# Kernel optimization log

Measured on AMD Instinct MI355X. Metric: run time of the kernel, lower is better.

The kernel has to match this reference:

```python
import jax, jax.numpy as jnp
import numpy as np

B, NB, K, L, S, V = 32, 688, 4, 688, 688, 50
PAD = 0
TEMP = 0.1
SMOOTH = 0.1
L_CLS, L_PTR, L_EMPTY, L_ROW, L_COL = 1.0, 1.0, 1.0, 0.5, 0.5


def setup_inputs() -> dict:
    key = jax.random.key(0)
    ks = jax.random.split(key, 12)
    tag_logits = jax.random.normal(ks[0], (B, S, V), jnp.float32)
    tag_targets = jax.random.randint(ks[1], (B, S), 0, V)
    pointer_logits = jax.random.normal(ks[2], (B, NB, S), jnp.float32)
    # targets only on even OTSL positions (which we mark as data tags below)
    raw = jax.random.randint(ks[3], (B, NB, K), 0, S // 2) * 2
    drop = jax.random.uniform(ks[4], (B, NB, K)) < 0.25
    box_indices = jnp.where(drop, -1, raw)
    pos = jnp.arange(S)
    data_otsl = jnp.broadcast_to(pos % 2 == 0, (B, S))
    empty_otsl = (pos % 2 == 1)[None, :] & (jax.random.uniform(ks[5], (B, S)) < 0.5)
    zeros_prompt = jnp.zeros((B, L), bool)
    data_tag_mask = jnp.concatenate([zeros_prompt, data_otsl], axis=1)
    empty_tag_mask = jnp.concatenate([zeros_prompt, empty_otsl], axis=1)
    empty_pointer_logits = jax.random.normal(ks[6], (B, 1, S), jnp.float32)
    row_sim_matrix = jax.random.normal(ks[7], (B, NB, NB), jnp.float32)
    col_sim_matrix = jax.random.normal(ks[8], (B, NB, NB), jnp.float32)

    def make_coef(k):
        k1, k2 = jax.random.split(k)
        c = jax.random.uniform(k1, (B, NB, NB))
        inv = jax.random.uniform(k2, (B, NB, NB)) < 0.1
        return jnp.where(inv, -1.0, c)

    row_span_coef = make_coef(ks[9])
    col_span_coef = make_coef(ks[10])
    return dict(tag_logits=tag_logits, tag_targets=tag_targets,
                pointer_logits=pointer_logits, box_indices=box_indices,
                data_tag_mask=data_tag_mask, empty_tag_mask=empty_tag_mask,
                empty_pointer_logits=empty_pointer_logits,
                row_sim_matrix=row_sim_matrix, col_sim_matrix=col_sim_matrix,
                row_span_coef=row_span_coef, col_span_coef=col_span_coef)


def _tag_loss(tag_logits, tag_targets):
    logp = jax.nn.log_softmax(tag_logits, axis=-1).reshape(-1, V)
    t = tag_targets.reshape(-1)
    valid = t != PAD
    nll = -jnp.take_along_axis(logp, jnp.where(valid, t, 0)[:, None], axis=1)[:, 0]
    smooth = -logp.mean(axis=-1)
    per = (1.0 - SMOOTH) * nll + SMOOTH * smooth
    return (per * valid).sum() / valid.sum()


def _pointer_loss(pointer_logits, box_indices, data_tag_mask):
    log_probs = jax.nn.log_softmax(pointer_logits / TEMP, axis=-1)  # (B,NB,S)
    valid_pos = data_tag_mask[:, L:]  # (B,S)
    log_probs = jnp.where(valid_pos[:, None, :], log_probs, -jnp.inf)
    valid = box_indices != -1  # (B,NB,K)
    safe = jnp.where(valid, box_indices, 0)
    g = jnp.take_along_axis(log_probs, safe, axis=-1)  # (B,NB,K)
    g = jnp.where(valid, g, 0.0)
    cnt = valid.sum(axis=-1)  # (B,NB)
    has = cnt > 0
    per = -(g.sum(axis=-1) / jnp.maximum(cnt, 1))
    total = (per * has).sum()
    return total / (has.sum() + 1e-6)


def _empty_ptr_loss(empty_logits, data_tag_mask, empty_tag_mask):
    x = empty_logits[:, 0, :]  # (B,S)
    otsl_mask = (data_tag_mask | empty_tag_mask)[:, L:]
    targets = empty_tag_mask[:, L:].astype(jnp.float32)
    # stable BCE with logits
    bce = jnp.maximum(x, 0.0) - x * targets + jnp.log1p(jnp.exp(-jnp.abs(x)))
    masked = bce * otsl_mask
    num_c = otsl_mask.sum(axis=1) + 1e-08
    return (masked.sum(axis=1) / num_c).mean()


def _contrastive_loss(sim, coef):
    s = sim / TEMP
    e = jnp.exp(s)
    lp = jnp.log(e / e.sum(axis=-1, keepdims=True) + 1e-08)
    vm = coef >= 0
    w = coef * lp * vm
    box = -(w.sum(axis=-1) / (coef.sum(axis=-1) + 1e-08))
    vb = vm.any(axis=-1)
    return (box * vb).sum() / (vb.sum() + 1e-08)


def reference(tag_logits, tag_targets, pointer_logits, box_indices,
              data_tag_mask, empty_tag_mask, empty_pointer_logits,
              row_sim_matrix, col_sim_matrix, row_span_coef, col_span_coef):
    cls_loss = _tag_loss(tag_logits, tag_targets)
    ptr_loss = _pointer_loss(pointer_logits, box_indices, data_tag_mask)
    empty_loss = _empty_ptr_loss(empty_pointer_logits, data_tag_mask, empty_tag_mask)
    row_loss = _contrastive_loss(row_sim_matrix, row_span_coef)
    col_loss = _contrastive_loss(col_sim_matrix, col_span_coef)
    total = (L_CLS * cls_loss + L_PTR * ptr_loss + L_EMPTY * empty_loss
             + L_ROW * row_loss + L_COL * col_loss)
    return (total, cls_loss, ptr_loss, empty_loss, row_loss, col_loss)
```

## Files before the change

### kernel.cpp

```cpp
#include <hip/hip_runtime.h>
#include <cstddef>

namespace {

constexpr int B  = 32;
constexpr int NB = 688;
constexpr int K  = 4;
constexpr int L  = 688;
constexpr int S  = 688;
constexpr int V  = 50;
constexpr int LS = L + S;
constexpr int ROWS = B * NB;
constexpr float TINV = 10.0f;
constexpr int Q3 = S / 4 - 128;
constexpr int QR = S / 4;

constexpr int NBLK  = 1024;
constexpr int NWAVE = NBLK * 4;

constexpr int A_PT = 0, A_PH = 1, A_RS = 2, A_RV = 3, A_CS = 4,
              A_CV = 5, A_TS = 6, A_TC = 7, A_ES = 8;

__device__ __forceinline__ float wred_sum(float v) {
#pragma unroll
  for (int o = 32; o > 0; o >>= 1) v += __shfl_xor(v, o);
  return v;
}
__device__ __forceinline__ void wred2(float& a, float& b) {
#pragma unroll
  for (int o = 32; o > 0; o >>= 1) { a += __shfl_xor(a, o); b += __shfl_xor(b, o); }
}
__device__ __forceinline__ void wred4(float& a, float& b, float& c, float& d) {
#pragma unroll
  for (int o = 32; o > 0; o >>= 1) {
    a += __shfl_xor(a, o); b += __shfl_xor(b, o);
    c += __shfl_xor(c, o); d += __shfl_xor(d, o);
  }
}

__device__ __forceinline__ float4 q_exp_t(const float4 v) {
  return make_float4(__expf(v.x * TINV), __expf(v.y * TINV),
                     __expf(v.z * TINV), __expf(v.w * TINV));
}
__device__ __forceinline__ float q_sum(const float4 a) {
  return (a.x + a.y) + (a.z + a.w);
}

__device__ __forceinline__ void load3(const float4* __restrict__ p4, int lane,
                                      bool t3, float4& a, float4& b, float4& c) {
  a = p4[lane];
  b = p4[lane + 64];
  c = t3 ? p4[lane + 128] : make_float4(0.f, 0.f, 0.f, 0.f);
}

__device__ __forceinline__ void c_quad(const float4 e, const float4 c,
                                       float A, float lgz,
                                       float& wsum, float& csum, bool& anyv) {
  csum += ((c.x + c.y) + (c.z + c.w));
  if (c.x >= 0.f) { wsum += c.x * (__logf(e.x + A) - lgz); anyv = true; }
  if (c.y >= 0.f) { wsum += c.y * (__logf(e.y + A) - lgz); anyv = true; }
  if (c.z >= 0.f) { wsum += c.z * (__logf(e.z + A) - lgz); anyv = true; }
  if (c.w >= 0.f) { wsum += c.w * (__logf(e.w + A) - lgz); anyv = true; }
}

__device__ __forceinline__ void ptr_row(int r, int lane, bool t3,
    const float* __restrict__ plog, const int* __restrict__ box,
    const int* __restrict__ dmask, float& a0, float& a1)
{
  const float*  pl  = plog + (size_t)r * S;
  const float4* pl4 = reinterpret_cast<const float4*>(pl);
  float4 v0, v1, v2;
  load3(pl4, lane, t3, v0, v1, v2);
  int idx = (lane < K) ? box[(size_t)r * K + lane] : -1;

  float4 e0 = q_exp_t(v0);
  float4 e1 = q_exp_t(v1);
  float4 e2 = t3 ? q_exp_t(v2) : make_float4(0.f, 0.f, 0.f, 0.f);
  float z = q_sum(e0) + q_sum(e1) + q_sum(e2);
  z = wred_sum(z);
  float lse = __logf(z);

  bool vld = (idx != -1) & (lane < K);
  float g = 0.f;
  if (vld) {
    int bb = r / NB;
    int vp = dmask[(size_t)bb * LS + L + idx];
    float sv = pl[idx] * TINV;
    g = vp ? (sv - lse) : -INFINITY;
  }
  g += __shfl_xor(g, 1);
  g += __shfl_xor(g, 2);
  unsigned long long bal = __ballot(vld);
  int cnt = __popcll(bal);
  if (cnt > 0) {
    a0 += -(g / (float)cnt);
    a1 += 1.f;
  }
}

__device__ __forceinline__ void tag_row(int row, int lane,
    const float* __restrict__ tl_base, const int* __restrict__ tgt,
    float& a0, float& a1)
{
  const float* tl = tl_base + (size_t)row * V;
  const bool a = (lane < V);
  float xv = a ? tl[lane] : 0.f;
  int   t  = tgt[row];
  float ev = a ? __expf(xv) : 0.f;
  float sx = a ? xv : 0.f;
  wred2(ev, sx);
  float lse = __logf(ev);
  float xt  = __shfl(xv, t);
  if (t != 0) {
    a0 += lse - 0.9f * xt - 0.002f * sx;
    a1 += 1.f;
  }
}

__device__ __forceinline__ void empty_row(int b, int lane,
    const float* __restrict__ elog, const int* __restrict__ dmask,
    const int* __restrict__ emask, float& a0)
{
  const float* el = elog + (size_t)b * S;
  const int* dm = dmask + (size_t)b * LS + L;
  const int* em = emask + (size_t)b * LS + L;
  float bs = 0.f, bc = 0.f;
  for (int j = lane; j < S; j += 64) {
    float xv = el[j];
    int d = dm[j], e = em[j];
    float tt = (float)e;
    float bce = fmaxf(xv, 0.f) - xv * tt + log1pf(__expf(-fabsf(xv)));
    if (d | e) { bs += bce; bc += 1.f; }
  }
  wred2(bs, bc);
  a0 += bs / (bc + 1e-8f);
}

__global__ __launch_bounds__(256, 4) void fused_loss(
    const float* __restrict__ tag_logits, const int* __restrict__ tag_targets,
    const float* __restrict__ plog, const int* __restrict__ box,
    const int* __restrict__ dmask, const int* __restrict__ emask,
    const float* __restrict__ elog,
    const float* __restrict__ rsim, const float* __restrict__ csim,
    const float* __restrict__ rcoef, const float* __restrict__ ccoef,
    float* __restrict__ ws)
{
  const int tid  = threadIdx.x;
  const int lane = tid & 63;
  const int wave = tid >> 6;
  const int wid  = blockIdx.x * 4 + wave;
  const bool t3  = (lane < Q3);

  const int ws_ = (wid * 43) >> 3;
  const int we_ = ((wid + 1) * 43) >> 3;

  float aPT = 0.f, aPH = 0.f, aRS = 0.f, aRV = 0.f, aCS = 0.f,
        aCV = 0.f, aTS = 0.f, aTC = 0.f, aES = 0.f;

  {
    float4 nr0, nr1, nr2, nm0, nm1, nm2;
    int r = ws_;
    if (r < we_) {
      load3(reinterpret_cast<const float4*>(rsim) + (size_t)r * QR, lane, t3, nr0, nr1, nr2);
      load3(reinterpret_cast<const float4*>(csim) + (size_t)r * QR, lane, t3, nm0, nm1, nm2);
    }
    while (r < we_) {
      float4 x0 = nr0, x1 = nr1, x2 = nr2;
      float4 y0 = nm0, y1 = nm1, y2 = nm2;
      float4 cr0, cr1, cr2, cm0, cm1, cm2;
      load3(reinterpret_cast<const float4*>(rcoef) + (size_t)r * QR, lane, t3, cr0, cr1, cr2);
      load3(reinterpret_cast<const float4*>(ccoef) + (size_t)r * QR, lane, t3, cm0, cm1, cm2);
      const int rn = r + 1;
      if (rn < we_) {
        load3(reinterpret_cast<const float4*>(rsim) + (size_t)rn * QR, lane, t3, nr0, nr1, nr2);
        load3(reinterpret_cast<const float4*>(csim) + (size_t)rn * QR, lane, t3, nm0, nm1, nm2);
      }
      x0 = q_exp_t(x0); x1 = q_exp_t(x1);
      x2 = t3 ? q_exp_t(x2) : make_float4(0.f, 0.f, 0.f, 0.f);
      y0 = q_exp_t(y0); y1 = q_exp_t(y1);
      y2 = t3 ? q_exp_t(y2) : make_float4(0.f, 0.f, 0.f, 0.f);

      float zr = q_sum(x0) + q_sum(x1) + q_sum(x2);
      float zc = q_sum(y0) + q_sum(y1) + q_sum(y2);
      wred2(zr, zc);
      const float Ar = 1e-8f * zr, lgzr = __logf(zr);
      const float Ac = 1e-8f * zc, lgzc = __logf(zc);

      float wr = 0.f, cr = 0.f, wc = 0.f, cc = 0.f;
      bool anyr = false, anyc = false;
      c_quad(x0, cr0, Ar, lgzr, wr, cr, anyr);
      c_quad(y0, cm0, Ac, lgzc, wc, cc, anyc);
      c_quad(x1, cr1, Ar, lgzr, wr, cr, anyr);
      c_quad(y1, cm1, Ac, lgzc, wc, cc, anyc);
      if (t3) {
        c_quad(x2, cr2, Ar, lgzr, wr, cr, anyr);
        c_quad(y2, cm2, Ac, lgzc, wc, cc, anyc);
      }
      wred4(wr, cr, wc, cc);
      if (__ballot(anyr)) { aRS += -(wr / (cr + 1e-8f)); aRV += 1.f; }
      if (__ballot(anyc)) { aCS += -(wc / (cc + 1e-8f)); aCV += 1.f; }
      r = rn;
    }
  }

  for (int r = ws_; r < we_; ++r) {
    ptr_row(r, lane, t3, plog, box, dmask, aPT, aPH);
    tag_row(r, lane, tag_logits, tag_targets, aTS, aTC);
  }

  if (wid < B) empty_row(wid, lane, elog, dmask, emask, aES);

  if (lane == 0) {
    ws[A_PT * NWAVE + wid] = aPT;
    ws[A_PH * NWAVE + wid] = aPH;
    ws[A_RS * NWAVE + wid] = aRS;
    ws[A_RV * NWAVE + wid] = aRV;
    ws[A_CS * NWAVE + wid] = aCS;
    ws[A_CV * NWAVE + wid] = aCV;
    ws[A_TS * NWAVE + wid] = aTS;
    ws[A_TC * NWAVE + wid] = aTC;
    ws[A_ES * NWAVE + wid] = aES;
  }
}

__global__ __launch_bounds__(256) void combine_kernel(
    const float* __restrict__ ws, float* __restrict__ out)
{
  const int tid  = threadIdx.x;
  const int lane = tid & 63;
  const int w    = tid >> 6;
  double acc[9];
#pragma unroll
  for (int a = 0; a < 9; ++a) acc[a] = 0.0;
  for (int i = tid; i < NWAVE; i += 256) {
#pragma unroll
    for (int a = 0; a < 9; ++a) acc[a] += (double)ws[a * NWAVE + i];
  }
#pragma unroll
  for (int a = 0; a < 9; ++a) {
#pragma unroll
    for (int o = 32; o > 0; o >>= 1) acc[a] += __shfl_xor(acc[a], o);
  }
  __shared__ double sh[4][9];
  if (lane == 0) {
#pragma unroll
    for (int a = 0; a < 9; ++a) sh[w][a] = acc[a];
  }
  __syncthreads();
  if (tid == 0) {
    double t[9];
#pragma unroll
    for (int a = 0; a < 9; ++a) t[a] = sh[0][a] + sh[1][a] + sh[2][a] + sh[3][a];
    float cls  = (float)(t[A_TS] / t[A_TC]);
    float ptr  = (float)(t[A_PT] / (t[A_PH] + 1e-6));
    float emp  = (float)(t[A_ES] / (double)B);
    float row  = (float)(t[A_RS] / (t[A_RV] + 1e-8));
    float col  = (float)(t[A_CS] / (t[A_CV] + 1e-8));
    float total = cls + ptr + emp + 0.5f * row + 0.5f * col;
    out[0] = total; out[1] = cls; out[2] = ptr;
    out[3] = emp;   out[4] = row; out[5] = col;
  }
}

}

extern "C" void kernel_launch(void* const* d_in, const int* in_sizes, int n_in,
                              void* d_out, int out_size, void* d_ws, size_t ws_size,
                              hipStream_t stream)
{
  const float* tag_logits  = (const float*)d_in[0];
  const int*   tag_targets = (const int*)  d_in[1];
  const float* plog        = (const float*)d_in[2];
  const int*   box         = (const int*)  d_in[3];
  const int*   dmask       = (const int*)  d_in[4];
  const int*   emask       = (const int*)  d_in[5];
  const float* elog        = (const float*)d_in[6];
  const float* rsim        = (const float*)d_in[7];
  const float* csim        = (const float*)d_in[8];
  const float* rcoef       = (const float*)d_in[9];
  const float* ccoef       = (const float*)d_in[10];

  float* ws  = (float*)d_ws;
  float* out = (float*)d_out;

  fused_loss<<<NBLK, 256, 0, stream>>>(tag_logits, tag_targets, plog, box,
                                       dmask, emask, elog, rsim, csim,
                                       rcoef, ccoef, ws);
  combine_kernel<<<1, 256, 0, stream>>>(ws, out);
}
```

Measured before the change: 72.37 us.

## Software-pipeline pointer/tag rows, use nontemporal loads and exp2, reduce per block

Fuses the pointer and tag row loops into one loop that prefetches the next row's pointer logits, box indices and tag logits while computing the current row, and merges their wave reductions into a single three-way shuffle reduction. The contrastive loads become nontemporal, and exp(x*10) is computed as exp2 with a folded constant. Per-wave partials are now summed in shared memory and written once per block, which shrinks the workspace the combine kernel reads. The prefetching raises register pressure, and the per-block reduction adds a block-wide barrier.

```diff
diff --git a/kernel.cpp b/kernel.cpp
--- a/kernel.cpp
+++ b/kernel.cpp
@@ -10,25 +10,32 @@
 constexpr int S  = 688;
 constexpr int V  = 50;
 constexpr int LS = L + S;
-constexpr int ROWS = B * NB;
 constexpr float TINV = 10.0f;
+constexpr float E10  = 14.4269504088896340736f;
 constexpr int Q3 = S / 4 - 128;
 constexpr int QR = S / 4;
 
 constexpr int NBLK  = 1024;
 constexpr int NWAVE = NBLK * 4;
 
+typedef float f32x4 __attribute__((ext_vector_type(4)));
+
 constexpr int A_PT = 0, A_PH = 1, A_RS = 2, A_RV = 3, A_CS = 4,
               A_CV = 5, A_TS = 6, A_TC = 7, A_ES = 8;
 
-__device__ __forceinline__ float wred_sum(float v) {
-#pragma unroll
-  for (int o = 32; o > 0; o >>= 1) v += __shfl_xor(v, o);
-  return v;
+__device__ __forceinline__ f32x4 zero4() {
+  f32x4 z = {0.f, 0.f, 0.f, 0.f};
+  return z;
 }
 __device__ __forceinline__ void wred2(float& a, float& b) {
 #pragma unroll
   for (int o = 32; o > 0; o >>= 1) { a += __shfl_xor(a, o); b += __shfl_xor(b, o); }
+}
+__device__ __forceinline__ void wred3(float& a, float& b, float& c) {
+#pragma unroll
+  for (int o = 32; o > 0; o >>= 1) {
+    a += __shfl_xor(a, o); b += __shfl_xor(b, o); c += __shfl_xor(c, o);
+  }
 }
 __device__ __forceinline__ void wred4(float& a, float& b, float& c, float& d) {
 #pragma unroll
@@ -38,22 +45,25 @@
   }
 }
 
-__device__ __forceinline__ float4 q_exp_t(const float4 v) {
-  return make_float4(__expf(v.x * TINV), __expf(v.y * TINV),
-                     __expf(v.z * TINV), __expf(v.w * TINV));
-}
-__device__ __forceinline__ float q_sum(const float4 a) {
+__device__ __forceinline__ f32x4 q_exp10(const f32x4 v) {
+  f32x4 r;
+  r.x = exp2f(v.x * E10); r.y = exp2f(v.y * E10);
+  r.z = exp2f(v.z * E10); r.w = exp2f(v.w * E10);
+  return r;
+}
+__device__ __forceinline__ float q_sum(const f32x4 a) {
   return (a.x + a.y) + (a.z + a.w);
 }
 
-__device__ __forceinline__ void load3(const float4* __restrict__ p4, int lane,
-                                      bool t3, float4& a, float4& b, float4& c) {
-  a = p4[lane];
-  b = p4[lane + 64];
-  c = t3 ? p4[lane + 128] : make_float4(0.f, 0.f, 0.f, 0.f);
-}
-
-__device__ __forceinline__ void c_quad(const float4 e, const float4 c,
+__device__ __forceinline__ void load3nt(const f32x4* __restrict__ p4, int lane,
+                                        bool t3, f32x4& a, f32x4& b, f32x4& c) {
+  a = __builtin_nontemporal_load(p4 + lane);
+  b = __builtin_nontemporal_load(p4 + lane + 64);
+  c = zero4();
+  if (t3) c = __builtin_nontemporal_load(p4 + lane + 128);
+}
+
+__device__ __forceinline__ void c_quad(const f32x4 e, const f32x4 c,
                                        float A, float lgz,
                                        float& wsum, float& csum, bool& anyv) {
   csum += ((c.x + c.y) + (c.z + c.w));
@@ -61,60 +71,6 @@
   if (c.y >= 0.f) { wsum += c.y * (__logf(e.y + A) - lgz); anyv = true; }
   if (c.z >= 0.f) { wsum += c.z * (__logf(e.z + A) - lgz); anyv = true; }
   if (c.w >= 0.f) { wsum += c.w * (__logf(e.w + A) - lgz); anyv = true; }
-}
-
-__device__ __forceinline__ void ptr_row(int r, int lane, bool t3,
-    const float* __restrict__ plog, const int* __restrict__ box,
-    const int* __restrict__ dmask, float& a0, float& a1)
-{
-  const float*  pl  = plog + (size_t)r * S;
-  const float4* pl4 = reinterpret_cast<const float4*>(pl);
-  float4 v0, v1, v2;
-  load3(pl4, lane, t3, v0, v1, v2);
-  int idx = (lane < K) ? box[(size_t)r * K + lane] : -1;
-
-  float4 e0 = q_exp_t(v0);
-  float4 e1 = q_exp_t(v1);
-  float4 e2 = t3 ? q_exp_t(v2) : make_float4(0.f, 0.f, 0.f, 0.f);
-  float z = q_sum(e0) + q_sum(e1) + q_sum(e2);
-  z = wred_sum(z);
-  float lse = __logf(z);
-
-  bool vld = (idx != -1) & (lane < K);
-  float g = 0.f;
-  if (vld) {
-    int bb = r / NB;
-    int vp = dmask[(size_t)bb * LS + L + idx];
-    float sv = pl[idx] * TINV;
-    g = vp ? (sv - lse) : -INFINITY;
-  }
-  g += __shfl_xor(g, 1);
-  g += __shfl_xor(g, 2);
-  unsigned long long bal = __ballot(vld);
-  int cnt = __popcll(bal);
-  if (cnt > 0) {
-    a0 += -(g / (float)cnt);
-    a1 += 1.f;
-  }
-}
-
-__device__ __forceinline__ void tag_row(int row, int lane,
-    const float* __restrict__ tl_base, const int* __restrict__ tgt,
-    float& a0, float& a1)
-{
-  const float* tl = tl_base + (size_t)row * V;
-  const bool a = (lane < V);
-  float xv = a ? tl[lane] : 0.f;
-  int   t  = tgt[row];
-  float ev = a ? __expf(xv) : 0.f;
-  float sx = a ? xv : 0.f;
-  wred2(ev, sx);
-  float lse = __logf(ev);
-  float xt  = __shfl(xv, t);
-  if (t != 0) {
-    a0 += lse - 0.9f * xt - 0.002f * sx;
-    a1 += 1.f;
-  }
 }
 
 __device__ __forceinline__ void empty_row(int b, int lane,
@@ -158,27 +114,27 @@
         aCV = 0.f, aTS = 0.f, aTC = 0.f, aES = 0.f;
 
   {
-    float4 nr0, nr1, nr2, nm0, nm1, nm2;
+    f32x4 nr0, nr1, nr2, nm0, nm1, nm2;
     int r = ws_;
     if (r < we_) {
-      load3(reinterpret_cast<const float4*>(rsim) + (size_t)r * QR, lane, t3, nr0, nr1, nr2);
-      load3(reinterpret_cast<const float4*>(csim) + (size_t)r * QR, lane, t3, nm0, nm1, nm2);
+      load3nt(reinterpret_cast<const f32x4*>(rsim) + (size_t)r * QR, lane, t3, nr0, nr1, nr2);
+      load3nt(reinterpret_cast<const f32x4*>(csim) + (size_t)r * QR, lane, t3, nm0, nm1, nm2);
     }
     while (r < we_) {
-      float4 x0 = nr0, x1 = nr1, x2 = nr2;
-      float4 y0 = nm0, y1 = nm1, y2 = nm2;
-      float4 cr0, cr1, cr2, cm0, cm1, cm2;
-      load3(reinterpret_cast<const float4*>(rcoef) + (size_t)r * QR, lane, t3, cr0, cr1, cr2);
-      load3(reinterpret_cast<const float4*>(ccoef) + (size_t)r * QR, lane, t3, cm0, cm1, cm2);
+      f32x4 x0 = nr0, x1 = nr1, x2 = nr2;
+      f32x4 y0 = nm0, y1 = nm1, y2 = nm2;
+      f32x4 cr0, cr1, cr2, cm0, cm1, cm2;
+      load3nt(reinterpret_cast<const f32x4*>(rcoef) + (size_t)r * QR, lane, t3, cr0, cr1, cr2);
+      load3nt(reinterpret_cast<const f32x4*>(ccoef) + (size_t)r * QR, lane, t3, cm0, cm1, cm2);
       const int rn = r + 1;
       if (rn < we_) {
-        load3(reinterpret_cast<const float4*>(rsim) + (size_t)rn * QR, lane, t3, nr0, nr1, nr2);
-        load3(reinterpret_cast<const float4*>(csim) + (size_t)rn * QR, lane, t3, nm0, nm1, nm2);
-      }
-      x0 = q_exp_t(x0); x1 = q_exp_t(x1);
-      x2 = t3 ? q_exp_t(x2) : make_float4(0.f, 0.f, 0.f, 0.f);
-      y0 = q_exp_t(y0); y1 = q_exp_t(y1);
-      y2 = t3 ? q_exp_t(y2) : make_float4(0.f, 0.f, 0.f, 0.f);
+        load3nt(reinterpret_cast<const f32x4*>(rsim) + (size_t)rn * QR, lane, t3, nr0, nr1, nr2);
+        load3nt(reinterpret_cast<const f32x4*>(csim) + (size_t)rn * QR, lane, t3, nm0, nm1, nm2);
+      }
+      x0 = q_exp10(x0); x1 = q_exp10(x1);
+      x2 = t3 ? q_exp10(x2) : zero4();
+      y0 = q_exp10(y0); y1 = q_exp10(y1);
+      y2 = t3 ? q_exp10(y2) : zero4();
 
       float zr = q_sum(x0) + q_sum(x1) + q_sum(x2);
       float zc = q_sum(y0) + q_sum(y1) + q_sum(y2);
@@ -203,23 +159,73 @@
     }
   }
 
-  for (int r = ws_; r < we_; ++r) {
-    ptr_row(r, lane, t3, plog, box, dmask, aPT, aPH);
-    tag_row(r, lane, tag_logits, tag_targets, aTS, aTC);
+  {
+    f32x4 np0, np1, np2;
+    float ntg; int nidx, ntt;
+    int r = ws_;
+    if (r < we_) {
+      const f32x4* pl4 = reinterpret_cast<const f32x4*>(plog) + (size_t)r * QR;
+      np0 = pl4[lane]; np1 = pl4[lane + 64];
+      np2 = zero4(); if (t3) np2 = pl4[lane + 128];
+      nidx = (lane < K) ? box[(size_t)r * K + lane] : -1;
+      ntg  = (lane < V) ? tag_logits[(size_t)r * V + lane] : 0.f;
+      ntt  = tag_targets[r];
+    }
+    while (r < we_) {
+      f32x4 p0 = np0, p1 = np1, p2 = np2;
+      float tg = ntg; int idx = nidx, tt = ntt;
+      const int rn = r + 1;
+      if (rn < we_) {
+        const f32x4* pl4 = reinterpret_cast<const f32x4*>(plog) + (size_t)rn * QR;
+        np0 = pl4[lane]; np1 = pl4[lane + 64];
+        np2 = zero4(); if (t3) np2 = pl4[lane + 128];
+        nidx = (lane < K) ? box[(size_t)rn * K + lane] : -1;
+        ntg  = (lane < V) ? tag_logits[(size_t)rn * V + lane] : 0.f;
+        ntt  = tag_targets[rn];
+      }
+      f32x4 e0 = q_exp10(p0), e1 = q_exp10(p1);
+      f32x4 e2 = t3 ? q_exp10(p2) : zero4();
+      float z  = q_sum(e0) + q_sum(e1) + q_sum(e2);
+      float ev = (lane < V) ? __expf(tg) : 0.f;
+      float sx = (lane < V) ? tg : 0.f;
+      wred3(z, ev, sx);
+      float lse = __logf(z);
+
+      bool vld = (idx != -1) & (lane < K);
+      float g = 0.f;
+      if (vld) {
+        int bb = r / NB;
+        int vp = dmask[(size_t)bb * LS + L + idx];
+        float sv = plog[(size_t)r * S + idx] * TINV;
+        g = vp ? (sv - lse) : -INFINITY;
+      }
+      g += __shfl_xor(g, 1);
+      g += __shfl_xor(g, 2);
+      int cnt = __popcll(__ballot(vld));
+      if (cnt > 0) { aPT += -(g / (float)cnt); aPH += 1.f; }
+
+      float tlse = __logf(ev);
+      float xt   = __shfl(tg, tt);
+      if (tt != 0) {
+        aTS += tlse - 0.9f * xt - 0.002f * sx;
+        aTC += 1.f;
+      }
+      r = rn;
+    }
   }
 
   if (wid < B) empty_row(wid, lane, elog, dmask, emask, aES);
 
+  __shared__ float sacc[4][9];
   if (lane == 0) {
-    ws[A_PT * NWAVE + wid] = aPT;
-    ws[A_PH * NWAVE + wid] = aPH;
-    ws[A_RS * NWAVE + wid] = aRS;
-    ws[A_RV * NWAVE + wid] = aRV;
-    ws[A_CS * NWAVE + wid] = aCS;
-    ws[A_CV * NWAVE + wid] = aCV;
-    ws[A_TS * NWAVE + wid] = aTS;
-    ws[A_TC * NWAVE + wid] = aTC;
-    ws[A_ES * NWAVE + wid] = aES;
+    sacc[wave][0] = aPT; sacc[wave][1] = aPH; sacc[wave][2] = aRS;
+    sacc[wave][3] = aRV; sacc[wave][4] = aCS; sacc[wave][5] = aCV;
+    sacc[wave][6] = aTS; sacc[wave][7] = aTC; sacc[wave][8] = aES;
+  }
+  __syncthreads();
+  if (tid < 9) {
+    float t0 = sacc[0][tid] + sacc[1][tid] + sacc[2][tid] + sacc[3][tid];
+    ws[tid * NBLK + blockIdx.x] = t0;
   }
 }
 
@@ -232,9 +238,9 @@
   double acc[9];
 #pragma unroll
   for (int a = 0; a < 9; ++a) acc[a] = 0.0;
-  for (int i = tid; i < NWAVE; i += 256) {
-#pragma unroll
-    for (int a = 0; a < 9; ++a) acc[a] += (double)ws[a * NWAVE + i];
+  for (int i = tid; i < NBLK; i += 256) {
+#pragma unroll
+    for (int a = 0; a < 9; ++a) acc[a] += (double)ws[a * NBLK + i];
   }
 #pragma unroll
   for (int a = 0; a < 9; ++a) {
```

Result: faster. 67.06 us (-7.3%).
